# Kernel tuning notes

Hardware: AMD Instinct MI355X
Metric: run time of the kernel (lower is better)

## Reference

```python
import jax, jax.numpy as jnp
import numpy as np

B, C, H, W = 16, 256, 56, 56
WH, WW = 7, 7
NH = 8            # heads
HID = 1024        # mlp hidden = int(4*dim)
N = WH * WW
EPS = 1e-5


def _rel_index():
    # mirrors the torch buffer computation in Rel_Attention.__init__
    coords = np.stack(np.meshgrid(np.arange(WH), np.arange(WW), indexing='ij')).reshape(2, -1)  # (2, N)
    rel = coords[:, :, None] - coords[:, None, :]  # (2, N, N)
    rel[0] += WH - 1
    rel[1] += WW - 1
    rel[0] *= 2 * WW - 1
    return jnp.asarray(rel.sum(0).reshape(-1))  # (N*N,)

REL_IDX = _rel_index()


def channel_ln(x, w, b):
    # LayerNorm over channel dim of NCHW tensor (permute -> LN -> permute back)
    xt = x.transpose(0, 2, 3, 1)  # BHWC
    mu = xt.mean(-1, keepdims=True)
    var = xt.var(-1, keepdims=True)
    xt = (xt - mu) / jnp.sqrt(var + EPS) * w + b
    return xt.transpose(0, 3, 1, 2)


def to_blocks(x):
    # (B,C,H,W) -> (B, H/wh, W/ww, C, wh, ww)
    b, c, h, w = x.shape
    x = x.reshape(b, c, h // WH, WH, w // WW, WW)
    return x.transpose(0, 2, 4, 1, 3, 5)


def unblock(x):
    # faithful to original: reshape(B, C, Hb*win_W, Hb*win_W)  (square sizes)
    b, hb, wb, c, wh, ww = x.shape
    return x.transpose(0, 3, 1, 4, 2, 5).reshape(b, c, hb * ww, hb * ww)


def rel_attention(xw, qkv_w, qkv_b, proj_w, proj_b, table):
    b, hb, wb, c = xw.shape[:4]
    hd = c // NH
    scale = hd ** (-0.5)
    xf = xw.reshape(-1, c, N)                                  # (M, C, N)
    qkv = jnp.einsum('oc,mcn->mon', qkv_w, xf) + qkv_b[None, :, None]
    q, k, v = jnp.split(qkv, 3, axis=1)

    def heads(t):
        return t.reshape(-1, NH, hd, N).transpose(0, 1, 3, 2)  # (M, h, N, d)

    q, k, v = heads(q), heads(k), heads(v)
    bias = table[REL_IDX].reshape(N, N, NH).transpose(2, 0, 1)  # (h, N, N)
    attn = jnp.einsum('mhnd,mhkd->mhnk', q, k) * scale + bias
    attn = jax.nn.softmax(attn, axis=-1)
    o = jnp.einsum('mhnk,mhkd->mhnd', attn, v)                 # (M, h, N, d)
    o = o.transpose(0, 1, 3, 2).reshape(-1, c, N)              # (M, C, N)
    o = jnp.einsum('oc,mcn->mon', proj_w, o) + proj_b[None, :, None]
    return o.reshape(b, hb, wb, c, WH, WW)


def mlp(x, fc1_w, fc1_b, fc2_w, fc2_b):
    h = jnp.einsum('oc,bchw->bohw', fc1_w, x) + fc1_b[None, :, None, None]
    h = jax.nn.gelu(h, approximate=False)
    return jnp.einsum('oc,bchw->bohw', fc2_w, h) + fc2_b[None, :, None, None]


def setup_inputs() -> dict:
    key = jax.random.key(0)
    ks = jax.random.split(key, 8)
    s = 0.02
    return {
        'x': jax.random.normal(ks[0], (B, C, H, W), jnp.float32),
        'ln1_w': jnp.ones((C,), jnp.float32),
        'ln1_b': jnp.zeros((C,), jnp.float32),
        'ln2_w': jnp.ones((C,), jnp.float32),
        'ln2_b': jnp.zeros((C,), jnp.float32),
        'qkv_w': jax.random.normal(ks[1], (3 * C, C), jnp.float32) * s,
        'qkv_b': jnp.zeros((3 * C,), jnp.float32),
        'proj_w': jax.random.normal(ks[2], (C, C), jnp.float32) * s,
        'proj_b': jnp.zeros((C,), jnp.float32),
        'rel_bias_table': jax.random.normal(ks[3], ((2 * WH - 1) * (2 * WW - 1), NH), jnp.float32) * s,
        'fc1_w': jax.random.normal(ks[4], (HID, C), jnp.float32) * s,
        'fc1_b': jnp.zeros((HID,), jnp.float32),
        'fc2_w': jax.random.normal(ks[5], (C, HID), jnp.float32) * s,
        'fc2_b': jnp.zeros((C,), jnp.float32),
    }


def reference(x, ln1_w, ln1_b, ln2_w, ln2_b, qkv_w, qkv_b, proj_w, proj_b,
              rel_bias_table, fc1_w, fc1_b, fc2_w, fc2_b):
    out = to_blocks(channel_ln(x, ln1_w, ln1_b))
    out = rel_attention(out, qkv_w, qkv_b, proj_w, proj_b, rel_bias_table)
    # original applies attn a second time before unblocking
    out = rel_attention(out, qkv_w, qkv_b, proj_w, proj_b, rel_bias_table)
    x = x + unblock(out)
    x = x + mlp(channel_ln(x, ln2_w, ln2_b), fc1_w, fc1_b, fc2_w, fc2_b)
    return x
```

## Files before the change

### kernel.cpp

```cpp
#include <hip/hip_runtime.h>
#include <stdint.h>

typedef uint16_t u16;
typedef short bf16x8 __attribute__((ext_vector_type(8)));
typedef float f32x4 __attribute__((ext_vector_type(4)));

__device__ __forceinline__ float bf2f(u16 s) {
  union { unsigned int i; float f; } c; c.i = ((unsigned int)s) << 16; return c.f;
}
__device__ __forceinline__ u16 f2bf(float f) {
  union { float f; unsigned int i; } c; c.f = f;
  unsigned int u = c.i;
  u += 0x7FFFu + ((u >> 16) & 1u);
  return (u16)(u >> 16);
}
__device__ __forceinline__ f32x4 mfma16(bf16x8 a, bf16x8 b, f32x4 c) {
  return __builtin_amdgcn_mfma_f32_16x16x32_bf16(a, b, c, 0, 0, 0);
}
__device__ __forceinline__ int dtype_flag(const u16* ln1w_raw) { return ln1w_raw[0] == 0x3F80 ? 1 : 0; }
__device__ __forceinline__ float loadF(const void* p, size_t i, int flag) {
  return flag ? bf2f(((const u16*)p)[i]) : ((const float*)p)[i];
}

#define OFF_QKVW 0
#define OFF_QKVB 196608
#define OFF_PROJW 197376
#define OFF_PROJB 262912
#define OFF_REL 263168
#define OFF_FC1W 264520
#define OFF_FC1B 526664
#define OFF_FC2W 527688
#define OFF_FC2B 789832
#define OFF_LN1W 790088
#define OFF_LN1B 790344
#define OFF_LN2W 790600
#define OFF_LN2B 790856
#define WC_TOTAL 791112

__global__ __launch_bounds__(256) void k_convert(const u16* __restrict__ ln1w_raw,
    const void* qkvw, const void* qkvb, const void* projw, const void* projb,
    const void* rel, const void* fc1w, const void* fc1b, const void* fc2w, const void* fc2b,
    const void* ln1w, const void* ln1b, const void* ln2w, const void* ln2b,
    u16* __restrict__ dst) {
  const int flag = dtype_flag(ln1w_raw);
  int i = blockIdx.x * 256 + threadIdx.x;
  if (i >= WC_TOTAL) return;
  const void* src; int off;
  if      (i < OFF_QKVB)  { src = qkvw;  off = i - OFF_QKVW; }
  else if (i < OFF_PROJW) { src = qkvb;  off = i - OFF_QKVB; }
  else if (i < OFF_PROJB) { src = projw; off = i - OFF_PROJW; }
  else if (i < OFF_REL)   { src = projb; off = i - OFF_PROJB; }
  else if (i < OFF_FC1W)  { src = rel;   off = i - OFF_REL; }
  else if (i < OFF_FC1B)  { src = fc1w;  off = i - OFF_FC1W; }
  else if (i < OFF_FC2W)  { src = fc1b;  off = i - OFF_FC1B; }
  else if (i < OFF_FC2B)  { src = fc2w;  off = i - OFF_FC2W; }
  else if (i < OFF_LN1W)  { src = fc2b;  off = i - OFF_FC2B; }
  else if (i < OFF_LN1B)  { src = ln1w;  off = i - OFF_LN1W; }
  else if (i < OFF_LN2W)  { src = ln1b;  off = i - OFF_LN1B; }
  else if (i < OFF_LN2B)  { src = ln2w;  off = i - OFF_LN2W; }
  else                    { src = ln2b;  off = i - OFF_LN2B; }
  if (i < OFF_QKVB) {
    int j = off & 7, li = (off >> 3) & 63, c0i = (off >> 9) & 7, grp = off >> 12;
    off = (grp * 16 + (li & 15)) * 256 + c0i * 32 + (li >> 4) * 8 + j;
  } else if (i >= OFF_PROJW && i < OFF_PROJB) {
    int j = off & 7, li = (off >> 3) & 63, c0i = (off >> 9) & 7, grp = off >> 12;
    off = (grp * 16 + (li & 15)) * 256 + c0i * 32 + (li >> 4) * 8 + j;
  } else if (i >= OFF_FC1W && i < OFF_FC1B) {
    int j = off & 7, li = (off >> 3) & 63, hj = (off >> 9) & 1, c0i = (off >> 10) & 7,
        w = (off >> 13) & 3, ch = off >> 15;
    off = (ch * 128 + w * 32 + hj * 16 + (li & 15)) * 256 + c0i * 32 + (li >> 4) * 8 + j;
  } else if (i >= OFF_FC2W && i < OFF_FC2B) {
    int j = off & 7, li = (off >> 3) & 63, oct = (off >> 9) & 3, kki = (off >> 11) & 3,
        ch = (off >> 13) & 7, w = off >> 16;
    off = (w * 64 + oct * 16 + (li & 15)) * 1024 + ch * 128 + kki * 32 + (li >> 4) * 8 + j;
  }
  dst[i] = flag ? ((const u16*)src)[off] : f2bf(((const float*)src)[off]);
}

__global__ __launch_bounds__(256) void k_ln1b(const void* __restrict__ xin,
                                              const u16* __restrict__ ln1w_raw,
                                              const u16* __restrict__ lw,
                                              const u16* __restrict__ lb,
                                              u16* __restrict__ win) {
  const int flag = dtype_flag(ln1w_raw);
  __shared__ float tile[56 * 257];
  __shared__ float smu[56], srs[56];
  const int bid = blockIdx.x;
  const int b = bid / 56, h = bid - b * 56;
  const int t = threadIdx.x;
  const int hb = h / 7, ph = h - hb * 7;
  {
    const int lane = t & 63, wq = t >> 6;
    if (lane < 56) {
#pragma unroll 4
      for (int ci = 0; ci < 64; ++ci) {
        const int c = ci * 4 + wq;
        const size_t addr = ((size_t)(b * 256 + c) * 56 + h) * 56 + lane;
        tile[lane * 257 + c] = loadF(xin, addr, flag);
      }
    }
  }
  __syncthreads();
  {
    const int row = t >> 2, qq = t & 3;
    float s = 0.f, q = 0.f;
    if (row < 56) {
      const float* tr = &tile[row * 257 + qq];
#pragma unroll 8
      for (int c0 = 0; c0 < 64; ++c0) { float v = tr[c0 * 4]; s += v; q += v * v; }
    }
    s += __shfl_xor(s, 1, 64); q += __shfl_xor(q, 1, 64);
    s += __shfl_xor(s, 2, 64); q += __shfl_xor(q, 2, 64);
    if (row < 56 && qq == 0) {
      float mm = s * (1.f / 256.f);
      float var = q * (1.f / 256.f) - mm * mm;
      smu[row] = mm; srs[row] = rsqrtf(var + 1e-5f);
    }
  }
  __syncthreads();
#pragma unroll
  for (int i = 0; i < 7; ++i) {
    int eid8 = i * 256 + t;
    int wp = eid8 >> 5, c8 = (eid8 & 31) << 3;
    const float mm = smu[wp], rs = srs[wp];
    const int m = b * 64 + hb * 8 + (wp / 7), n = ph * 7 + (wp % 7);
    bf16x8 o;
#pragma unroll
    for (int j = 0; j < 8; ++j) {
      int c = c8 + j;
      o[j] = (short)f2bf((tile[wp * 257 + c] - mm) * rs * bf2f(lw[c]) + bf2f(lb[c]));
    }
    *(bf16x8*)&win[(size_t)m * 12544 + n * 256 + c8] = o;
  }
}

__global__ __launch_bounds__(512) void k_attn_stage(const u16* __restrict__ win,
                                                    const u16* __restrict__ qkvw,
                                                    const u16* __restrict__ qkvb,
                                                    const u16* __restrict__ rel,
                                                    const u16* __restrict__ projw,
                                                    const u16* __restrict__ projb,
                                                    u16* __restrict__ wout) {
  __shared__ __align__(16) u16 xs[64 * 264];
  __shared__ __align__(16) u16 wa[8][7424];
  const int m = blockIdx.x;
  const int t = threadIdx.x;
  const int w = t >> 6, li = t & 63, lane = li & 15, quad = li >> 4;
  const int hg = w;
  const f32x4 z = {0.f, 0.f, 0.f, 0.f};
  const u16* src = win + (size_t)m * 12544;
#pragma unroll
  for (int i = 0; i < 4; ++i) {
    int chunk = i * 512 + t;
    if (chunk < 1568) {
      int n = chunk >> 5, cc = (chunk & 31) << 3;
      *(bf16x8*)&xs[n * 264 + cc] = *(const bf16x8*)&src[chunk << 3];
    }
  }
  for (int i = t; i < 15 * 264; i += 512) xs[49 * 264 + i] = 0;
  u16* qw = wa[w];
  u16* kw = wa[w] + 2560;
  u16* vw = wa[w] + 5120;
  u16* Pw = wa[w];
  u16* Os = xs;
  for (int i = li; i < 15 * 40; i += 64) { qw[49 * 40 + i] = 0; kw[49 * 40 + i] = 0; }
  for (int i = li; i < 32 * 15; i += 64) { int d = i / 15, j = i - d * 15; vw[d * 72 + 49 + j] = 0; }
  __syncthreads();
  const float SCALE = 0.17677669529663687f;
#pragma unroll
  for (int part = 0; part < 2; ++part) {
    const int obase = part * 256 + hg * 32;
    f32x4 acc[4][2];
#pragma unroll
    for (int i = 0; i < 4; ++i) { acc[i][0] = z; acc[i][1] = z; }
#pragma unroll
    for (int c0i = 0; c0i < 8; ++c0i) {
      bf16x8 a[4], b[2];
#pragma unroll
      for (int nt = 0; nt < 4; ++nt)
        a[nt] = *(const bf16x8*)&xs[(nt * 16 + lane) * 264 + c0i * 32 + quad * 8];
#pragma unroll
      for (int oj = 0; oj < 2; ++oj)
        b[oj] = *(const bf16x8*)&qkvw[(size_t)(((part * 16 + hg * 2 + oj) * 8 + c0i) * 64 + li) * 8];
#pragma unroll
      for (int nt = 0; nt < 4; ++nt)
#pragma unroll
        for (int oj = 0; oj < 2; ++oj) acc[nt][oj] = mfma16(a[nt], b[oj], acc[nt][oj]);
    }
    u16* dstL = part ? kw : qw;
#pragma unroll
    for (int oj = 0; oj < 2; ++oj) {
      const int d = oj * 16 + lane;
      const float bias = bf2f(qkvb[obase + d]);
#pragma unroll
      for (int nt = 0; nt < 4; ++nt)
#pragma unroll
        for (int r = 0; r < 4; ++r) {
          int n = nt * 16 + quad * 4 + r;
          if (n < 49) dstL[n * 40 + d] = f2bf(acc[nt][oj][r] + bias);
        }
    }
  }
  {
    f32x4 acc[2][4];
#pragma unroll
    for (int i = 0; i < 2; ++i)
#pragma unroll
      for (int j = 0; j < 4; ++j) acc[i][j] = z;
#pragma unroll
    for (int c0i = 0; c0i < 8; ++c0i) {
      bf16x8 a[2], b[4];
#pragma unroll
      for (int vj = 0; vj < 2; ++vj)
        a[vj] = *(const bf16x8*)&qkvw[(size_t)(((32 + hg * 2 + vj) * 8 + c0i) * 64 + li) * 8];
#pragma unroll
      for (int nt = 0; nt < 4; ++nt)
        b[nt] = *(const bf16x8*)&xs[(nt * 16 + lane) * 264 + c0i * 32 + quad * 8];
#pragma unroll
      for (int vj = 0; vj < 2; ++vj)
#pragma unroll
        for (int nt = 0; nt < 4; ++nt) acc[vj][nt] = mfma16(a[vj], b[nt], acc[vj][nt]);
    }
#pragma unroll
    for (int vj = 0; vj < 2; ++vj)
#pragma unroll
      for (int r = 0; r < 4; ++r) {
        const int d = vj * 16 + quad * 4 + r;
        const float bias = bf2f(qkvb[512 + hg * 32 + d]);
#pragma unroll
        for (int nt = 0; nt < 4; ++nt) {
          int n = nt * 16 + lane;
          if (n < 49) vw[d * 72 + n] = f2bf(acc[vj][nt][r] + bias);
        }
      }
  }
  __syncthreads();
  f32x4 s[4][4];
  {
    bf16x8 aq[4], bk[4];
#pragma unroll
    for (int nt = 0; nt < 4; ++nt) {
      aq[nt] = *(const bf16x8*)&qw[(nt * 16 + lane) * 40 + quad * 8];
      bk[nt] = *(const bf16x8*)&kw[(nt * 16 + lane) * 40 + quad * 8];
    }
#pragma unroll
    for (int i = 0; i < 4; ++i)
#pragma unroll
      for (int j = 0; j < 4; ++j) s[i][j] = mfma16(aq[i], bk[j], z);
  }
#pragma unroll
  for (int nt1 = 0; nt1 < 4; ++nt1) {
#pragma unroll
    for (int r = 0; r < 4; ++r) {
      int n1 = nt1 * 16 + quad * 4 + r;
      int n1c = n1 < 49 ? n1 : 48;
      int ph1 = n1c / 7, pw1 = n1c - ph1 * 7;
      float v[4];
#pragma unroll
      for (int j = 0; j < 4; ++j) {
        int n2 = j * 16 + lane;
        if (n2 < 49) {
          int ph2 = n2 / 7, pw2 = n2 - ph2 * 7;
          int idx = (ph1 - ph2 + 6) * 13 + (pw1 - pw2 + 6);
          v[j] = s[nt1][j][r] * SCALE + bf2f(rel[idx * 8 + hg]);
        } else v[j] = -1e30f;
      }
      float mx = fmaxf(fmaxf(v[0], v[1]), fmaxf(v[2], v[3]));
      for (int off = 1; off < 16; off <<= 1) mx = fmaxf(mx, __shfl_xor(mx, off, 64));
      float e0 = __expf(v[0] - mx), e1 = __expf(v[1] - mx);
      float e2 = __expf(v[2] - mx), e3 = __expf(v[3] - mx);
      float sum = e0 + e1 + e2 + e3;
      for (int off = 1; off < 16; off <<= 1) sum += __shfl_xor(sum, off, 64);
      float rinv = __builtin_amdgcn_rcpf(sum);
      Pw[n1 * 72 + 0 * 16 + lane] = f2bf(e0 * rinv);
      Pw[n1 * 72 + 1 * 16 + lane] = f2bf(e1 * rinv);
      Pw[n1 * 72 + 2 * 16 + lane] = f2bf(e2 * rinv);
      Pw[n1 * 72 + 3 * 16 + lane] = f2bf(e3 * rinv);
    }
  }
  {
    f32x4 o[4][2];
#pragma unroll
    for (int i = 0; i < 4; ++i) { o[i][0] = z; o[i][1] = z; }
#pragma unroll
    for (int kc = 0; kc < 2; ++kc) {
      bf16x8 ap[4], bv[2];
#pragma unroll
      for (int nt1 = 0; nt1 < 4; ++nt1)
        ap[nt1] = *(const bf16x8*)&Pw[(nt1 * 16 + lane) * 72 + kc * 32 + quad * 8];
#pragma unroll
      for (int dt = 0; dt < 2; ++dt)
        bv[dt] = *(const bf16x8*)&vw[(dt * 16 + lane) * 72 + kc * 32 + quad * 8];
#pragma unroll
      for (int nt1 = 0; nt1 < 4; ++nt1)
#pragma unroll
        for (int dt = 0; dt < 2; ++dt) o[nt1][dt] = mfma16(ap[nt1], bv[dt], o[nt1][dt]);
    }
#pragma unroll
    for (int nt1 = 0; nt1 < 4; ++nt1)
#pragma unroll
      for (int dt = 0; dt < 2; ++dt)
#pragma unroll
        for (int r = 0; r < 4; ++r) {
          int n1 = nt1 * 16 + quad * 4 + r;
          if (n1 < 49) Os[n1 * 264 + hg * 32 + dt * 16 + lane] = f2bf(o[nt1][dt][r]);
        }
  }
  __syncthreads();
  {
    f32x4 acc[4][2];
#pragma unroll
    for (int i = 0; i < 4; ++i) { acc[i][0] = z; acc[i][1] = z; }
#pragma unroll
    for (int c0i = 0; c0i < 8; ++c0i) {
      bf16x8 a[4], b[2];
#pragma unroll
      for (int nt = 0; nt < 4; ++nt)
        a[nt] = *(const bf16x8*)&Os[(nt * 16 + lane) * 264 + c0i * 32 + quad * 8];
#pragma unroll
      for (int oj = 0; oj < 2; ++oj)
        b[oj] = *(const bf16x8*)&projw[(size_t)(((w * 2 + oj) * 8 + c0i) * 64 + li) * 8];
#pragma unroll
      for (int nt = 0; nt < 4; ++nt)
#pragma unroll
        for (int oj = 0; oj < 2; ++oj) acc[nt][oj] = mfma16(a[nt], b[oj], acc[nt][oj]);
    }
#pragma unroll
    for (int oj = 0; oj < 2; ++oj) {
      const int oc = w * 32 + oj * 16 + lane;
      const float bias = bf2f(projb[oc]);
#pragma unroll
      for (int nt = 0; nt < 4; ++nt)
#pragma unroll
        for (int r = 0; r < 4; ++r) {
          int n = nt * 16 + quad * 4 + r;
          if (n < 49) wout[(size_t)m * 12544 + n * 256 + oc] = f2bf(acc[nt][oj][r] + bias);
        }
    }
  }
}

__global__ __launch_bounds__(256) void k_resid2(const void* __restrict__ xin,
                                                const u16* __restrict__ ln1w_raw,
                                                const u16* __restrict__ attn,
                                                const u16* __restrict__ l2w,
                                                const u16* __restrict__ l2b,
                                                u16* __restrict__ xrn,
                                                u16* __restrict__ ln2d) {
  const int flag = dtype_flag(ln1w_raw);
  __shared__ float tile[56 * 257];
  __shared__ float smu[56], srs[56];
  const int bid = blockIdx.x;
  const int b = bid / 56, h = bid - b * 56;
  const int t = threadIdx.x;
  const int hb = h / 7, ph = h - hb * 7;
#pragma unroll
  for (int i = 0; i < 7; ++i) {
    int eid8 = i * 256 + t;
    int wp = eid8 >> 5, c8 = (eid8 & 31) << 3;
    int mm = b * 64 + hb * 8 + (wp / 7), nn = ph * 7 + (wp % 7);
    bf16x8 v = *(const bf16x8*)&attn[(size_t)mm * 12544 + nn * 256 + c8];
    float* dst = &tile[wp * 257 + c8];
#pragma unroll
    for (int j = 0; j < 8; ++j) dst[j] = bf2f((u16)v[j]);
  }
  __syncthreads();
  {
    const int lane = t & 63, wq = t >> 6;
    if (lane < 56) {
#pragma unroll 4
      for (int ci = 0; ci < 64; ++ci) {
        const int c = ci * 4 + wq;
        const size_t addr = ((size_t)(b * 256 + c) * 56 + h) * 56 + lane;
        float v = tile[lane * 257 + c] + loadF(xin, addr, flag);
        tile[lane * 257 + c] = v;
        xrn[addr] = f2bf(v);
      }
    }
  }
  __syncthreads();
  {
    const int row = t >> 2, qq = t & 3;
    float s = 0.f, q = 0.f;
    if (row < 56) {
      const float* tr = &tile[row * 257 + qq];
#pragma unroll 8
      for (int c0 = 0; c0 < 64; ++c0) { float v = tr[c0 * 4]; s += v; q += v * v; }
    }
    s += __shfl_xor(s, 1, 64); q += __shfl_xor(q, 1, 64);
    s += __shfl_xor(s, 2, 64); q += __shfl_xor(q, 2, 64);
    if (row < 56 && qq == 0) {
      float mm = s * (1.f / 256.f);
      float var = q * (1.f / 256.f) - mm * mm;
      smu[row] = mm; srs[row] = rsqrtf(var + 1e-5f);
    }
  }
  __syncthreads();
#pragma unroll
  for (int i = 0; i < 7; ++i) {
    int eid8 = i * 256 + t;
    int wp = eid8 >> 5, c8 = (eid8 & 31) << 3;
    const float mm = smu[wp], rs = srs[wp];
    bf16x8 o;
#pragma unroll
    for (int j = 0; j < 8; ++j) {
      int c = c8 + j;
      o[j] = (short)f2bf((tile[wp * 257 + c] - mm) * rs * bf2f(l2w[c]) + bf2f(l2b[c]));
    }
    *(bf16x8*)&ln2d[((size_t)b * 3136 + h * 56 + wp) * 256 + c8] = o;
  }
}

__global__ __launch_bounds__(256, 2) void k_mlp2(const u16* __restrict__ ln2d,
                                                 const u16* __restrict__ w1,
                                                 const u16* __restrict__ b1,
                                                 const u16* __restrict__ w2,
                                                 const u16* __restrict__ b2,
                                                 const u16* __restrict__ xrn,
                                                 const u16* __restrict__ ln1w_raw,
                                                 void* __restrict__ out) {
  const int flag = dtype_flag(ln1w_raw);
  __shared__ __align__(16) u16 arena[34304];
  u16* xp = arena;
  u16* g0 = arena + 16896;
  u16* g1 = arena + 25600;
  const int pix0 = blockIdx.x * 64;
  const int t = threadIdx.x;
  const int w = t >> 6, li = t & 63, lane = li & 15, quad = li >> 4;
#pragma unroll
  for (int i = 0; i < 8; ++i) {
    int eid8 = i * 256 + t;
    int row = eid8 >> 5, c8 = (eid8 & 31) << 3;
    *(bf16x8*)&xp[row * 264 + c8] = *(const bf16x8*)&ln2d[(size_t)(pix0 + row) * 256 + c8];
  }
  __syncthreads();
  const f32x4 z = {0.f, 0.f, 0.f, 0.f};
  f32x4 acc2[4][4];
#pragma unroll
  for (int i = 0; i < 4; ++i)
#pragma unroll
    for (int j = 0; j < 4; ++j) acc2[i][j] = z;

  auto fc1_load = [&](int ch, bf16x8 (&bw)[8][2]) {
#pragma unroll
    for (int c0i = 0; c0i < 8; ++c0i)
#pragma unroll
      for (int hj = 0; hj < 2; ++hj)
        bw[c0i][hj] = *(const bf16x8*)&w1[(size_t)((((ch * 4 + w) * 8 + c0i) * 2 + hj) * 64 + li) * 8];
  };
  auto fc1_fin = [&](int ch, bf16x8 (&bw)[8][2], u16* gdst) {
    f32x4 a1[4][2];
#pragma unroll
    for (int i = 0; i < 4; ++i) { a1[i][0] = z; a1[i][1] = z; }
#pragma unroll
    for (int c0i = 0; c0i < 8; ++c0i) {
      bf16x8 av[4];
#pragma unroll
      for (int pt = 0; pt < 4; ++pt)
        av[pt] = *(const bf16x8*)&xp[(pt * 16 + lane) * 264 + c0i * 32 + quad * 8];
#pragma unroll
      for (int pt = 0; pt < 4; ++pt)
#pragma unroll
        for (int hj = 0; hj < 2; ++hj) a1[pt][hj] = mfma16(av[pt], bw[c0i][hj], a1[pt][hj]);
    }
#pragma unroll
    for (int hj = 0; hj < 2; ++hj) {
      const int hl = w * 32 + hj * 16 + lane;
      const float bias = bf2f(b1[ch * 128 + hl]);
#pragma unroll
      for (int pt = 0; pt < 4; ++pt)
#pragma unroll
        for (int r = 0; r < 4; ++r) {
          float u_ = a1[pt][hj][r] + bias;
          float y = u_ * fmaf(u_ * u_, 0.035677408136300125f, 0.7978845608028654f);
          float e2 = __expf(-2.f * y);
          float v = u_ * __builtin_amdgcn_rcpf(1.f + e2);
          gdst[(pt * 16 + quad * 4 + r) * 136 + hl] = f2bf(v);
        }
    }
  };
  auto fc2 = [&](int ch, const u16* gsrc) {
#pragma unroll
    for (int kki = 0; kki < 4; ++kki) {
      bf16x8 aw[4], bg[4];
#pragma unroll
      for (int oct = 0; oct < 4; ++oct)
        aw[oct] = *(const bf16x8*)&w2[(size_t)((((w * 8 + ch) * 4 + kki) * 4 + oct) * 64 + li) * 8];
#pragma unroll
      for (int pt = 0; pt < 4; ++pt)
        bg[pt] = *(const bf16x8*)&gsrc[(pt * 16 + lane) * 136 + kki * 32 + quad * 8];
#pragma unroll
      for (int oct = 0; oct < 4; ++oct)
#pragma unroll
        for (int pt = 0; pt < 4; ++pt) acc2[oct][pt] = mfma16(aw[oct], bg[pt], acc2[oct][pt]);
    }
  };

  {
    bf16x8 bw[8][2];
    fc1_load(0, bw);
    fc1_fin(0, bw, g0);
  }
  __syncthreads();
#pragma unroll 1
  for (int ch = 0; ch < 7; ++ch) {
    bf16x8 bw[8][2];
    fc1_load(ch + 1, bw);
    fc2(ch, (ch & 1) ? g1 : g0);
    fc1_fin(ch + 1, bw, (ch & 1) ? g0 : g1);
    __syncthreads();
  }
  fc2(7, g1);

  __syncthreads();
  float* Ob = (float*)arena;
#pragma unroll
  for (int oct = 0; oct < 4; ++oct)
#pragma unroll
    for (int pt = 0; pt < 4; ++pt)
#pragma unroll
      for (int r = 0; r < 4; ++r)
        Ob[(w * 64 + oct * 16 + quad * 4 + r) * 65 + pt * 16 + lane] = acc2[oct][pt][r];
  __syncthreads();
  {
    const int b_ = pix0 / 3136, rem0 = pix0 - b_ * 3136;
    const int sub = t & 7;
    const int r0 = t >> 3;
    bf16x8 xr[8];
    size_t addrs[8];
#pragma unroll
    for (int i = 0; i < 8; ++i) {
      const int oc = i * 32 + r0;
      addrs[i] = (size_t)(b_ * 256 + oc) * 3136 + rem0 + sub * 8;
      xr[i] = *(const bf16x8*)&xrn[addrs[i]];
    }
#pragma unroll
    for (int i = 0; i < 8; ++i) {
      const int oc = i * 32 + r0;
      const float bias = bf2f(b2[oc]);
      const float* obr = &Ob[oc * 65 + sub * 8];
      float v[8];
#pragma unroll
      for (int j = 0; j < 8; ++j)
        v[j] = obr[j] + bias + bf2f((u16)xr[i][j]);
      if (flag) {
        bf16x8 o8;
#pragma unroll
        for (int j = 0; j < 8; ++j) o8[j] = (short)f2bf(v[j]);
        *(bf16x8*)&((u16*)out)[addrs[i]] = o8;
      } else {
        float* dst = &((float*)out)[addrs[i]];
        f32x4 lo = {v[0], v[1], v[2], v[3]}, hi = {v[4], v[5], v[6], v[7]};
        *(f32x4*)&dst[0] = lo;
        *(f32x4*)&dst[4] = hi;
      }
    }
  }
}

extern "C" void kernel_launch(void* const* d_in, const int* in_sizes, int n_in,
                              void* d_out, int out_size, void* d_ws, size_t ws_size,
                              hipStream_t stream) {
  (void)in_sizes; (void)n_in; (void)out_size; (void)ws_size;
  const void* x     = d_in[0];
  const u16* ln1w_raw = (const u16*)d_in[1];
  u16* ws = (u16*)d_ws;
  const size_t R = 12845056;
  u16* R0 = ws;
  u16* R1 = ws + R;
  u16* R2 = ws + 2 * R;
  u16* WC = ws + 3 * R;
  const u16* qkvw_c = WC + OFF_QKVW;
  const u16* qkvb_c = WC + OFF_QKVB;
  const u16* projw_c = WC + OFF_PROJW;
  const u16* projb_c = WC + OFF_PROJB;
  const u16* rel_c  = WC + OFF_REL;
  const u16* fc1w_c = WC + OFF_FC1W;
  const u16* fc1b_c = WC + OFF_FC1B;
  const u16* fc2w_c = WC + OFF_FC2W;
  const u16* fc2b_c = WC + OFF_FC2B;
  const u16* ln1w_c = WC + OFF_LN1W;
  const u16* ln1b_c = WC + OFF_LN1B;
  const u16* ln2w_c = WC + OFF_LN2W;
  const u16* ln2b_c = WC + OFF_LN2B;

  k_convert<<<(WC_TOTAL + 255) / 256, 256, 0, stream>>>(
      ln1w_raw, d_in[5], d_in[6], d_in[7], d_in[8], d_in[9],
      d_in[10], d_in[11], d_in[12], d_in[13], d_in[1], d_in[2], d_in[3], d_in[4], WC);

  k_ln1b      <<<896, 256, 0, stream>>>(x, ln1w_raw, ln1w_c, ln1b_c, R0);
  k_attn_stage<<<1024, 512, 0, stream>>>(R0, qkvw_c, qkvb_c, rel_c, projw_c, projb_c, R1);
  k_attn_stage<<<1024, 512, 0, stream>>>(R1, qkvw_c, qkvb_c, rel_c, projw_c, projb_c, R2);
  k_resid2    <<<896, 256, 0, stream>>>(x, ln1w_raw, R2, ln2w_c, ln2b_c, R0, R1);
  k_mlp2      <<<784, 256, 0, stream>>>(R1, fc1w_c, fc1b_c, fc2w_c, fc2b_c, R0, ln1w_raw, d_out);
}
```

Before: 513.4 us.

## Pre-swizzle LN2 output into MFMA fragment layout and halve MLP LDS footprint

The LN2 kernel now writes its output directly in the per-lane MFMA A-fragment order, so the MLP kernel reads A operands straight from global memory instead of staging the 64x256 activation tile in LDS. This removes the staging copy and barrier and roughly halves shared memory. Launch bounds go from 2 to 4 blocks per SM, and the output epilogue is split into two halves so the smaller arena can hold the transposed results. The trade-off is that A fragments are re-read from global/L2 for every hidden chunk, and the fc1 weight prefetch that previously overlapped fc2 is dropped.

```diff
diff --git a/kernel.cpp b/kernel.cpp
--- a/kernel.cpp
+++ b/kernel.cpp
@@ -407,11 +407,14 @@
       int c = c8 + j;
       o[j] = (short)f2bf((tile[wp * 257 + c] - mm) * rs * bf2f(l2w[c]) + bf2f(l2b[c]));
     }
-    *(bf16x8*)&ln2d[((size_t)b * 3136 + h * 56 + wp) * 256 + c8] = o;
-  }
-}
-
-__global__ __launch_bounds__(256, 2) void k_mlp2(const u16* __restrict__ ln2d,
+    const int p = b * 3136 + h * 56 + wp;
+    const int pblk = p >> 6, pt = (p & 63) >> 4, r16 = p & 15;
+    const int c0i = c8 >> 5, quad = (c8 >> 3) & 3;
+    *(bf16x8*)&ln2d[(size_t)((((pblk * 4 + pt) * 8 + c0i) * 64 + quad * 16 + r16)) << 3] = o;
+  }
+}
+
+__global__ __launch_bounds__(256, 4) void k_mlp2(const u16* __restrict__ aG,
                                                  const u16* __restrict__ w1,
                                                  const u16* __restrict__ b1,
                                                  const u16* __restrict__ w2,
@@ -420,20 +423,13 @@
                                                  const u16* __restrict__ ln1w_raw,
                                                  void* __restrict__ out) {
   const int flag = dtype_flag(ln1w_raw);
-  __shared__ __align__(16) u16 arena[34304];
-  u16* xp = arena;
-  u16* g0 = arena + 16896;
-  u16* g1 = arena + 25600;
-  const int pix0 = blockIdx.x * 64;
+  __shared__ __align__(16) u16 arena[17408];
+  u16* g0 = arena;
+  u16* g1 = arena + 8704;
+  const int pblk = blockIdx.x;
+  const int pix0 = pblk * 64;
   const int t = threadIdx.x;
   const int w = t >> 6, li = t & 63, lane = li & 15, quad = li >> 4;
-#pragma unroll
-  for (int i = 0; i < 8; ++i) {
-    int eid8 = i * 256 + t;
-    int row = eid8 >> 5, c8 = (eid8 & 31) << 3;
-    *(bf16x8*)&xp[row * 264 + c8] = *(const bf16x8*)&ln2d[(size_t)(pix0 + row) * 256 + c8];
-  }
-  __syncthreads();
   const f32x4 z = {0.f, 0.f, 0.f, 0.f};
   f32x4 acc2[4][4];
 #pragma unroll
@@ -441,27 +437,23 @@
 #pragma unroll
     for (int j = 0; j < 4; ++j) acc2[i][j] = z;
 
-  auto fc1_load = [&](int ch, bf16x8 (&bw)[8][2]) {
-#pragma unroll
-    for (int c0i = 0; c0i < 8; ++c0i)
+  auto fc1 = [&](int ch, u16* gdst) {
+    f32x4 a1[4][2];
+#pragma unroll
+    for (int i = 0; i < 4; ++i) { a1[i][0] = z; a1[i][1] = z; }
+#pragma unroll
+    for (int c0i = 0; c0i < 8; ++c0i) {
+      bf16x8 av[4], bw[2];
+#pragma unroll
+      for (int pt = 0; pt < 4; ++pt)
+        av[pt] = *(const bf16x8*)&aG[(size_t)((((pblk * 4 + pt) * 8 + c0i) * 64 + li)) * 8];
 #pragma unroll
       for (int hj = 0; hj < 2; ++hj)
-        bw[c0i][hj] = *(const bf16x8*)&w1[(size_t)((((ch * 4 + w) * 8 + c0i) * 2 + hj) * 64 + li) * 8];
-  };
-  auto fc1_fin = [&](int ch, bf16x8 (&bw)[8][2], u16* gdst) {
-    f32x4 a1[4][2];
-#pragma unroll
-    for (int i = 0; i < 4; ++i) { a1[i][0] = z; a1[i][1] = z; }
-#pragma unroll
-    for (int c0i = 0; c0i < 8; ++c0i) {
-      bf16x8 av[4];
+        bw[hj] = *(const bf16x8*)&w1[(size_t)((((ch * 4 + w) * 8 + c0i) * 2 + hj) * 64 + li) * 8];
 #pragma unroll
       for (int pt = 0; pt < 4; ++pt)
-        av[pt] = *(const bf16x8*)&xp[(pt * 16 + lane) * 264 + c0i * 32 + quad * 8];
-#pragma unroll
-      for (int pt = 0; pt < 4; ++pt)
-#pragma unroll
-        for (int hj = 0; hj < 2; ++hj) a1[pt][hj] = mfma16(av[pt], bw[c0i][hj], a1[pt][hj]);
+#pragma unroll
+        for (int hj = 0; hj < 2; ++hj) a1[pt][hj] = mfma16(av[pt], bw[hj], a1[pt][hj]);
     }
 #pragma unroll
     for (int hj = 0; hj < 2; ++hj) {
@@ -496,49 +488,46 @@
     }
   };
 
-  {
-    bf16x8 bw[8][2];
-    fc1_load(0, bw);
-    fc1_fin(0, bw, g0);
-  }
+  fc1(0, g0);
   __syncthreads();
 #pragma unroll 1
   for (int ch = 0; ch < 7; ++ch) {
-    bf16x8 bw[8][2];
-    fc1_load(ch + 1, bw);
     fc2(ch, (ch & 1) ? g1 : g0);
-    fc1_fin(ch + 1, bw, (ch & 1) ? g0 : g1);
+    fc1(ch + 1, (ch & 1) ? g0 : g1);
     __syncthreads();
   }
   fc2(7, g1);
 
-  __syncthreads();
   float* Ob = (float*)arena;
-#pragma unroll
-  for (int oct = 0; oct < 4; ++oct)
-#pragma unroll
-    for (int pt = 0; pt < 4; ++pt)
-#pragma unroll
-      for (int r = 0; r < 4; ++r)
-        Ob[(w * 64 + oct * 16 + quad * 4 + r) * 65 + pt * 16 + lane] = acc2[oct][pt][r];
-  __syncthreads();
-  {
-    const int b_ = pix0 / 3136, rem0 = pix0 - b_ * 3136;
-    const int sub = t & 7;
-    const int r0 = t >> 3;
-    bf16x8 xr[8];
-    size_t addrs[8];
-#pragma unroll
-    for (int i = 0; i < 8; ++i) {
-      const int oc = i * 32 + r0;
+  const int b_ = pix0 / 3136, rem0 = pix0 - b_ * 3136;
+  const int sub = t & 7, r0 = t >> 3;
+#pragma unroll 1
+  for (int e = 0; e < 2; ++e) {
+    __syncthreads();
+    if ((w >> 1) == e) {
+      const int wl = w & 1;
+#pragma unroll
+      for (int oct = 0; oct < 4; ++oct)
+#pragma unroll
+        for (int pt = 0; pt < 4; ++pt)
+#pragma unroll
+          for (int r = 0; r < 4; ++r)
+            Ob[(wl * 64 + oct * 16 + quad * 4 + r) * 65 + pt * 16 + lane] = acc2[oct][pt][r];
+    }
+    __syncthreads();
+    bf16x8 xr[4];
+    size_t addrs[4];
+#pragma unroll
+    for (int i = 0; i < 4; ++i) {
+      const int oc = e * 128 + i * 32 + r0;
       addrs[i] = (size_t)(b_ * 256 + oc) * 3136 + rem0 + sub * 8;
       xr[i] = *(const bf16x8*)&xrn[addrs[i]];
     }
 #pragma unroll
-    for (int i = 0; i < 8; ++i) {
-      const int oc = i * 32 + r0;
+    for (int i = 0; i < 4; ++i) {
+      const int oc = e * 128 + i * 32 + r0;
       const float bias = bf2f(b2[oc]);
-      const float* obr = &Ob[oc * 65 + sub * 8];
+      const float* obr = &Ob[(i * 32 + r0) * 65 + sub * 8];
       float v[8];
 #pragma unroll
       for (int j = 0; j < 8; ++j)
```

Result: slower. 687.2 us (+33.9%).
